# Optimization experiments

Hardware: AMD Instinct MI355X
Metric: run time of the kernel (lower is better)

The kernel has to match this reference:

```python
import jax, jax.numpy as jnp
import numpy as np

B, N, M = 4, 512, 8192
QUERY_DIM, INPUT_DIM = 512, 256
HEADS, DIM_HEAD = 8, 64
ATT_DIM = HEADS * DIM_HEAD  # 512


def setup_inputs() -> dict:
    key = jax.random.key(0)
    ks = jax.random.split(key, 6)
    x = jax.random.normal(ks[0], (B, N, QUERY_DIM), dtype=jnp.float32)
    context = jax.random.normal(ks[1], (B, M, INPUT_DIM), dtype=jnp.float32)
    # Linear weights stored as [in, out] for x @ W
    Wq = jax.random.normal(ks[2], (QUERY_DIM, ATT_DIM), dtype=jnp.float32) / np.sqrt(QUERY_DIM)
    Wkv = jax.random.normal(ks[3], (INPUT_DIM, 2 * ATT_DIM), dtype=jnp.float32) / np.sqrt(INPUT_DIM)
    Wo = jax.random.normal(ks[4], (ATT_DIM, QUERY_DIM), dtype=jnp.float32) / np.sqrt(ATT_DIM)
    bo = jax.random.normal(ks[5], (QUERY_DIM,), dtype=jnp.float32) * 0.01
    return {"x": x, "context": context, "Wq": Wq, "Wkv": Wkv, "Wo": Wo, "bo": bo}


def reference(x, context, Wq, Wkv, Wo, bo):
    scale = DIM_HEAD ** -0.5
    q = x @ Wq                      # [B, N, H*D]
    kv = context @ Wkv              # [B, M, 2*H*D]
    k, v = jnp.split(kv, 2, axis=-1)
    # split heads: b n (h d) -> b h n d
    q = q.reshape(B, N, HEADS, DIM_HEAD).transpose(0, 2, 1, 3)
    k = k.reshape(B, M, HEADS, DIM_HEAD).transpose(0, 2, 1, 3)
    v = v.reshape(B, M, HEADS, DIM_HEAD).transpose(0, 2, 1, 3)
    scores = jnp.einsum('bhid,bhjd->bhij', q, k) * scale  # [B, H, N, M]
    attn = jax.nn.softmax(scores, axis=-1)
    out = jnp.einsum('bhij,bhjd->bhid', attn, v)           # [B, H, N, D]
    out = out.transpose(0, 2, 1, 3).reshape(B, N, ATT_DIM)
    return out @ Wo + bo
```

## Files before the change

### kernel.cpp

```cpp
#include <hip/hip_runtime.h>
#include <hip/hip_bf16.h>
#include <cstdint>

#define NB 4
#define NQ 512
#define NM 8192
#define NH 8
#define DH 64

typedef short bf16x8s __attribute__((ext_vector_type(8)));
typedef float f32x4  __attribute__((ext_vector_type(4)));

static __device__ __forceinline__ short f2bs(float f) {
    unsigned u = __builtin_bit_cast(unsigned, f);
    return (short)(unsigned short)((u + 0x8000u) >> 16);
}
static __device__ __forceinline__ unsigned pk2(float a, float b) {
    unsigned au = __builtin_bit_cast(unsigned, a) + 0x8000u;
    unsigned bu = __builtin_bit_cast(unsigned, b) + 0x8000u;
    return __builtin_amdgcn_perm(bu, au, 0x07060302u);
}

#if __has_builtin(__builtin_amdgcn_exp2f)
static __device__ __forceinline__ float fexp2(float x) { return __builtin_amdgcn_exp2f(x); }
#else
static __device__ __forceinline__ float fexp2(float x) { return exp2f(x); }
#endif

__global__ __launch_bounds__(256) void prep_weights(
    const float* __restrict__ Wq, const float* __restrict__ Wo,
    const float* __restrict__ Wkv,
    short* __restrict__ Wqf, short* __restrict__ Wof, short* __restrict__ Wkvf)
{
    const int t = threadIdx.x;
    const int w = t >> 6, ln = t & 63;
    const int m16 = ln & 15, quad = ln >> 4;
    int f = blockIdx.x * 4 + w;
    const float* src; short* dst; int N, KS, n0, ks;
    if (f < 512)       { src = Wq;  dst = Wqf;  N = 512;  KS = 16; n0 = f >> 4; ks = f & 15; }
    else if (f < 1024) { f -= 512;  src = Wo;  dst = Wof;  N = 512;  KS = 16; n0 = f >> 4; ks = f & 15; }
    else               { f -= 1024; src = Wkv; dst = Wkvf; N = 1024; KS = 8;  n0 = f >> 3; ks = f & 7; }
    const float* sp = src + (size_t)(ks * 32 + quad * 8) * N + n0 * 16 + m16;
    float v[8];
    #pragma unroll
    for (int j = 0; j < 8; ++j) v[j] = sp[(size_t)j * N];
    uint4 pkv = { pk2(v[0],v[1]), pk2(v[2],v[3]), pk2(v[4],v[5]), pk2(v[6],v[7]) };
    *(uint4*)(dst + ((size_t)(n0 * KS + ks) * 64 + ln) * 8) = pkv;
}

__device__ __forceinline__ void proj32_body(
    const float* __restrict__ A, const short* __restrict__ Wf,
    float* __restrict__ C, const float* __restrict__ bias,
    int tm, int tn, char* smemraw)
{
    short* As = (short*)smemraw;

    const int t = threadIdx.x;
    const int w = t >> 6, ln = t & 63;
    const int m16 = ln & 15, quad = ln >> 4;
    const int wm = w >> 1, wn = w & 1;

    const int ar = t >> 3, ac = (t & 7) << 3;

    const float* Ap = A + (size_t)(tm * 32 + ar) * 512 + ac;

    f32x4 acc[2] = {};

    for (int k0 = 0; k0 < 512; k0 += 64) {
        float4 a0 = *(const float4*)(Ap + k0);
        float4 a1 = *(const float4*)(Ap + k0 + 4);
        bf16x8s bfr[2][2];
        #pragma unroll
        for (int ks = 0; ks < 2; ++ks)
            #pragma unroll
            for (int nt = 0; nt < 2; ++nt)
                bfr[ks][nt] = *(const bf16x8s*)(Wf +
                    ((size_t)((tn * 4 + wn * 2 + nt) * 16 + (k0 >> 5) + ks) * 64 + ln) * 8);

        __syncthreads();
        {
            uint4 wa = { pk2(a0.x,a0.y), pk2(a0.z,a0.w), pk2(a1.x,a1.y), pk2(a1.z,a1.w) };
            *(uint4*)&As[ar * 72 + ac] = wa;
        }
        __syncthreads();

        #pragma unroll
        for (int ks = 0; ks < 2; ++ks) {
            bf16x8s af = *(const bf16x8s*)&As[(wm * 16 + m16) * 72 + ks * 32 + quad * 8];
            #pragma unroll
            for (int nt = 0; nt < 2; ++nt)
                acc[nt] = __builtin_amdgcn_mfma_f32_16x16x32_bf16(af, bfr[ks][nt], acc[nt], 0, 0, 0);
        }
    }

    const int row0 = tm * 32 + wm * 16 + quad * 4;
    const int col0 = tn * 64 + wn * 32;
    #pragma unroll
    for (int nt = 0; nt < 2; ++nt) {
        const int col = col0 + nt * 16 + m16;
        const float bb = bias ? bias[col] : 0.f;
        #pragma unroll
        for (int r = 0; r < 4; ++r)
            C[(size_t)(row0 + r) * 512 + col] = acc[nt][r] + bb;
    }
}

__device__ __forceinline__ void kv_body(
    const float* __restrict__ A, const short* __restrict__ Wkvf,
    short* __restrict__ Kf, short* __restrict__ Vf,
    int bid, char* smemraw)
{
    short* As = (short*)smemraw;

    const int t  = threadIdx.x;
    const int tm = bid & 255, tn = bid >> 8;
    const int w  = t >> 6, ln = t & 63;
    const int m16 = ln & 15, quad = ln >> 4;
    const int wm = w & 1, wn = w >> 1;

    const int ar = t >> 3;
    const int ac = (t & 7) << 2;

    const float* Abase = A + (size_t)(tm * 128 + ar) * 256 + ac;

    f32x4 acc[4][4] = {};

    for (int k0 = 0; k0 < 256; k0 += 32) {
        float4 av[4];
        #pragma unroll
        for (int p = 0; p < 4; ++p)
            av[p] = *(const float4*)(Abase + (size_t)p * 32 * 256 + k0);
        bf16x8s bfr[4];
        #pragma unroll
        for (int j = 0; j < 4; ++j)
            bfr[j] = *(const bf16x8s*)(Wkvf +
                ((size_t)((tn * 8 + wn * 4 + j) * 8 + (k0 >> 5)) * 64 + ln) * 8);

        __syncthreads();
        #pragma unroll
        for (int p = 0; p < 4; ++p) {
            uint2 wv = { pk2(av[p].x, av[p].y), pk2(av[p].z, av[p].w) };
            *(uint2*)&As[(p * 32 + ar) * 40 + ac] = wv;
        }
        __syncthreads();

        bf16x8s af[4];
        #pragma unroll
        for (int i = 0; i < 4; ++i)
            af[i] = *(const bf16x8s*)&As[(wm * 64 + i * 16 + m16) * 40 + quad * 8];
        #pragma unroll
        for (int i = 0; i < 4; ++i)
            #pragma unroll
            for (int j = 0; j < 4; ++j)
                acc[i][j] = __builtin_amdgcn_mfma_f32_16x16x32_bf16(af[i], bfr[j], acc[i][j], 0, 0, 0);
    }

    const int col0 = tn * 128 + wn * 64;
    const int row0 = tm * 128 + wm * 64;
    const int b    = row0 >> 13;
    const int mr0  = row0 & (NM - 1);

    if (col0 < 512) {
        const int h = col0 >> 6;
        short* Kp = Kf + (size_t)(b * NH + h) * (NM * DH);
        #pragma unroll
        for (int i = 0; i < 4; ++i)
            #pragma unroll
            for (int j = 0; j < 4; ++j) {
                const int d = j * 16 + m16;
                #pragma unroll
                for (int r = 0; r < 4; ++r) {
                    const int key = mr0 + i * 16 + quad * 4 + r;
                    const int idx = ((key >> 4) * 2 + (d >> 5)) * 512
                                  + (((d >> 3) & 3) * 16 + (key & 15)) * 8 + (d & 7);
                    Kp[idx] = f2bs(acc[i][j][r]);
                }
            }
    } else {
        const int h = (col0 - 512) >> 6;
        short* Vp = Vf + (size_t)(b * NH + h) * (NM * DH);
        #pragma unroll
        for (int i = 0; i < 4; ++i)
            #pragma unroll
            for (int j = 0; j < 4; ++j) {
                const int key0 = mr0 + i * 16 + quad * 4;
                const int idx = (j * 256 + (key0 >> 5)) * 512
                              + ((((key0 >> 3) & 3) * 16 + m16) * 8) + (key0 & 7);
                uint2 pk;
                pk.x = pk2(acc[i][j][0], acc[i][j][1]);
                pk.y = pk2(acc[i][j][2], acc[i][j][3]);
                *(uint2*)(Vp + idx) = pk;
            }
    }
}

__global__ __launch_bounds__(256) void gemm_kvq(
    const float* __restrict__ x,   const short* __restrict__ Wqf, float* __restrict__ q,
    const float* __restrict__ ctx, const short* __restrict__ Wkvf,
    short* __restrict__ Kf, short* __restrict__ Vf)
{
    __shared__ __align__(16) char smem[10240];
    if (blockIdx.x < 512)
        proj32_body(x, Wqf, q, nullptr, (int)(blockIdx.x >> 3), (int)(blockIdx.x & 7), smem);
    else
        kv_body(ctx, Wkvf, Kf, Vf, (int)(blockIdx.x - 512), smem);
}

__global__ __launch_bounds__(256) void gemm_proj32(
    const float* __restrict__ A, const short* __restrict__ Wf,
    float* __restrict__ C, const float* __restrict__ bias)
{
    __shared__ __align__(16) char smem[32 * 72 * 2];
    proj32_body(A, Wf, C, bias, (int)(blockIdx.x >> 3), (int)(blockIdx.x & 7), smem);
}

__global__ __launch_bounds__(512, 2) void attn_mfma(
    const float* __restrict__ Q,
    const short* __restrict__ Kfr,
    const short* __restrict__ Vfr,
    float* __restrict__ Og)
{
    __shared__ __align__(16) float Ob[2][64 * 66];
    __shared__ float lbuf[8 * 64];

    const int bid = blockIdx.x;
    const int xcd = bid & 7, g = bid >> 3;
    const int bh  = xcd * 4 + (g & 3);
    const int qt  = g >> 2;
    const int b   = bh >> 3, h = bh & 7;
    const int t   = threadIdx.x;
    const int w   = t >> 6, ln = t & 63;
    const int m16 = ln & 15, quad = ln >> 4;

    const short* Kbase = Kfr + (size_t)bh * (NM * DH);
    const short* Vbase = Vfr + (size_t)bh * (NM * DH);

    const float qsc = 0.125f * 1.44269504f;
    bf16x8s qf[4][2];
    #pragma unroll
    for (int mt = 0; mt < 4; ++mt) {
        const float* qrow = Q + ((size_t)(b * NQ + qt * 64 + mt * 16 + m16)) * 512 + h * 64;
        #pragma unroll
        for (int ks = 0; ks < 2; ++ks) {
            float4 x0 = *(const float4*)(qrow + ks * 32 + quad * 8);
            float4 x1 = *(const float4*)(qrow + ks * 32 + quad * 8 + 4);
            uint4 pkv = { pk2(x0.x * qsc, x0.y * qsc), pk2(x0.z * qsc, x0.w * qsc),
                          pk2(x1.x * qsc, x1.y * qsc), pk2(x1.z * qsc, x1.w * qsc) };
            qf[mt][ks] = *reinterpret_cast<bf16x8s*>(&pkv);
        }
    }

    bf16x8s ones;
    #pragma unroll
    for (int j = 0; j < 8; ++j) ones[j] = (short)0x3F80;

    f32x4 o[4][4] = {};
    f32x4 lsum[4] = {};

    const int srcLo = (((quad << 1) & 3) << 4) + m16;
    const int srcHi = ((((quad << 1) + 1) & 3) << 4) + m16;
    const bool ktHi = quad >= 2;

    bf16x8s kf[4][2];
    {
        const int kc = w * 64;
        #pragma unroll
        for (int nt = 0; nt < 4; ++nt)
            #pragma unroll
            for (int ks = 0; ks < 2; ++ks)
                kf[nt][ks] = *(const bf16x8s*)(Kbase + ((((kc >> 4) + nt) * 2 + ks) << 9) + ln * 8);
    }

    for (int it = 0; it < 16; ++it) {
        const int kc = it * 512 + w * 64;

        bf16x8s vf[4][2];
        #pragma unroll
        for (int dt = 0; dt < 4; ++dt)
            #pragma unroll
            for (int ks = 0; ks < 2; ++ks)
                vf[dt][ks] = *(const bf16x8s*)(Vbase + ((dt * 256 + (kc >> 5) + ks) << 9) + ln * 8);

        f32x4 st[4][4] = {};
        #pragma unroll
        for (int kt = 0; kt < 4; ++kt)
            #pragma unroll
            for (int mt = 0; mt < 4; ++mt) {
                st[mt][kt] = __builtin_amdgcn_mfma_f32_16x16x32_bf16(kf[kt][0], qf[mt][0], st[mt][kt], 0, 0, 0);
                st[mt][kt] = __builtin_amdgcn_mfma_f32_16x16x32_bf16(kf[kt][1], qf[mt][1], st[mt][kt], 0, 0, 0);
            }

        if (it + 1 < 16) {
            const int kn = (it + 1) * 512 + w * 64;
            #pragma unroll
            for (int nt = 0; nt < 4; ++nt)
                #pragma unroll
                for (int ks = 0; ks < 2; ++ks)
                    kf[nt][ks] = *(const bf16x8s*)(Kbase + ((((kn >> 4) + nt) * 2 + ks) << 9) + ln * 8);
        }

        unsigned pp[4][4][2];
        #pragma unroll
        for (int mt = 0; mt < 4; ++mt)
            #pragma unroll
            for (int kt = 0; kt < 4; ++kt) {
                const float p0 = fexp2(st[mt][kt][0]);
                const float p1 = fexp2(st[mt][kt][1]);
                const float p2 = fexp2(st[mt][kt][2]);
                const float p3 = fexp2(st[mt][kt][3]);
                pp[mt][kt][0] = pk2(p0, p1);
                pp[mt][kt][1] = pk2(p2, p3);
            }

        #pragma unroll
        for (int mt = 0; mt < 4; ++mt)
            #pragma unroll
            for (int ks = 0; ks < 2; ++ks) {
                const unsigned a0 = __shfl(pp[mt][2 * ks][0], srcLo);
                const unsigned b0 = __shfl(pp[mt][2 * ks + 1][0], srcLo);
                const unsigned a1 = __shfl(pp[mt][2 * ks][1], srcLo);
                const unsigned b1 = __shfl(pp[mt][2 * ks + 1][1], srcLo);
                const unsigned a2 = __shfl(pp[mt][2 * ks][0], srcHi);
                const unsigned b2 = __shfl(pp[mt][2 * ks + 1][0], srcHi);
                const unsigned a3 = __shfl(pp[mt][2 * ks][1], srcHi);
                const unsigned b3 = __shfl(pp[mt][2 * ks + 1][1], srcHi);
                uint4 pb;
                pb.x = ktHi ? b0 : a0;
                pb.y = ktHi ? b1 : a1;
                pb.z = ktHi ? b2 : a2;
                pb.w = ktHi ? b3 : a3;
                bf16x8s pbv = *reinterpret_cast<bf16x8s*>(&pb);
                #pragma unroll
                for (int dt = 0; dt < 4; ++dt)
                    o[mt][dt] = __builtin_amdgcn_mfma_f32_16x16x32_bf16(vf[dt][ks], pbv, o[mt][dt], 0, 0, 0);
                lsum[mt] = __builtin_amdgcn_mfma_f32_16x16x32_bf16(ones, pbv, lsum[mt], 0, 0, 0);
            }
    }

    if (quad == 0) {
        #pragma unroll
        for (int mt = 0; mt < 4; ++mt)
            lbuf[w * 64 + mt * 16 + m16] = lsum[mt][0];
    }
    if (w < 2) {
        float* dst = Ob[w];
        #pragma unroll
        for (int mt = 0; mt < 4; ++mt)
            #pragma unroll
            for (int dt = 0; dt < 4; ++dt)
                *(f32x4*)&dst[(mt * 16 + m16) * 66 + dt * 16 + quad * 4] = o[mt][dt];
    }
    __syncthreads();
    #pragma unroll
    for (int ph = 1; ph < 4; ++ph) {
        if ((w >> 1) == ph) {
            float* dst = Ob[w & 1];
            #pragma unroll
            for (int mt = 0; mt < 4; ++mt)
                #pragma unroll
                for (int dt = 0; dt < 4; ++dt) {
                    float* p = &dst[(mt * 16 + m16) * 66 + dt * 16 + quad * 4];
                    f32x4 cur = *(f32x4*)p;
                    cur += o[mt][dt];
                    *(f32x4*)p = cur;
                }
        }
        __syncthreads();
    }
    {
        const int row = t >> 3;
        const int d0  = (t & 7) << 3;
        float l = 0.f;
        #pragma unroll
        for (int wi = 0; wi < 8; ++wi) l += lbuf[wi * 64 + row];
        const float inv = 1.0f / l;
        float* op = Og + ((size_t)(b * NQ + qt * 64 + row)) * 512 + h * 64 + d0;
        #pragma unroll
        for (int j = 0; j < 2; ++j) {
            const int c = row * 66 + d0 + j * 4;
            float4 r;
            r.x = (Ob[0][c + 0] + Ob[1][c + 0]) * inv;
            r.y = (Ob[0][c + 1] + Ob[1][c + 1]) * inv;
            r.z = (Ob[0][c + 2] + Ob[1][c + 2]) * inv;
            r.w = (Ob[0][c + 3] + Ob[1][c + 3]) * inv;
            *(float4*)(op + j * 4) = r;
        }
    }
}

extern "C" void kernel_launch(void* const* d_in, const int* in_sizes, int n_in,
                              void* d_out, int out_size, void* d_ws, size_t ws_size,
                              hipStream_t stream) {
    (void)in_sizes; (void)n_in; (void)out_size; (void)ws_size;

    const float* x   = (const float*)d_in[0];
    const float* ctx = (const float*)d_in[1];
    const float* Wq  = (const float*)d_in[2];
    const float* Wkv = (const float*)d_in[3];
    const float* Wo  = (const float*)d_in[4];
    const float* bo  = (const float*)d_in[5];
    float* out = (float*)d_out;

    float* ws    = (float*)d_ws;
    float* q     = ws;
    float* attno = q + (size_t)2048 * 512;
    short* Kf    = (short*)(attno + (size_t)2048 * 512);
    short* Vf    = Kf + (size_t)NB * NH * NM * DH;
    short* Wqf   = Vf + (size_t)NB * NH * NM * DH;
    short* Wof   = Wqf + (size_t)512 * 512;
    short* Wkvf  = Wof + (size_t)512 * 512;

    prep_weights<<<dim3(384), dim3(256), 0, stream>>>(Wq, Wo, Wkv, Wqf, Wof, Wkvf);

    gemm_kvq<<<dim3(2560), dim3(256), 0, stream>>>(x, Wqf, q, ctx, Wkvf, Kf, Vf);

    attn_mfma<<<dim3(256), dim3(512), 0, stream>>>(q, Kf, Vf, attno);

    gemm_proj32<<<dim3(512), dim3(256), 0, stream>>>(attno, Wof, out, bo);
}
```

Baseline: 189.6 us.

## Rearrange V layout to feed PV MFMAs directly, removing cross-lane shuffles

Changes the V buffer layout written by the KV projection so each lane's 16-bit-aligned score fragment from the QK MFMA output can feed a 16x16x16 bf16 MFMA directly, removing the 16 shuffles and selects per tile in the attention loop. V is stored and loaded as contiguous uint4 per lane, and the KV block index mapping is also reordered. In exchange, the PV product uses twice as many smaller-K MFMA instructions (16x16x16 instead of 16x16x32), which have lower throughput per instruction.

```diff
diff --git a/kernel.cpp b/kernel.cpp
--- a/kernel.cpp
+++ b/kernel.cpp
@@ -9,6 +9,7 @@
 #define DH 64
 
 typedef short bf16x8s __attribute__((ext_vector_type(8)));
+typedef short bf16x4s __attribute__((ext_vector_type(4)));
 typedef float f32x4  __attribute__((ext_vector_type(4)));
 
 static __device__ __forceinline__ short f2bs(float f) {
@@ -108,12 +109,13 @@
 __device__ __forceinline__ void kv_body(
     const float* __restrict__ A, const short* __restrict__ Wkvf,
     short* __restrict__ Kf, short* __restrict__ Vf,
-    int bid, char* smemraw)
+    int kvid, char* smemraw)
 {
     short* As = (short*)smemraw;
 
     const int t  = threadIdx.x;
-    const int tm = bid & 255, tn = bid >> 8;
+    const int tm = ((kvid >> 6) << 3) | (kvid & 7);
+    const int tn = (kvid >> 3) & 7;
     const int w  = t >> 6, ln = t & 63;
     const int m16 = ln & 15, quad = ln >> 4;
     const int wm = w & 1, wn = w >> 1;
@@ -180,16 +182,15 @@
         const int h = (col0 - 512) >> 6;
         short* Vp = Vf + (size_t)(b * NH + h) * (NM * DH);
         #pragma unroll
-        for (int i = 0; i < 4; ++i)
-            #pragma unroll
-            for (int j = 0; j < 4; ++j) {
-                const int key0 = mr0 + i * 16 + quad * 4;
-                const int idx = (j * 256 + (key0 >> 5)) * 512
-                              + ((((key0 >> 3) & 3) * 16 + m16) * 8) + (key0 & 7);
-                uint2 pk;
-                pk.x = pk2(acc[i][j][0], acc[i][j][1]);
-                pk.y = pk2(acc[i][j][2], acc[i][j][3]);
-                *(uint2*)(Vp + idx) = pk;
+        for (int j = 0; j < 4; ++j)
+            #pragma unroll
+            for (int p = 0; p < 2; ++p) {
+                uint4 v;
+                v.x = pk2(acc[2*p    ][j][0], acc[2*p    ][j][1]);
+                v.y = pk2(acc[2*p    ][j][2], acc[2*p    ][j][3]);
+                v.z = pk2(acc[2*p + 1][j][0], acc[2*p + 1][j][1]);
+                v.w = pk2(acc[2*p + 1][j][2], acc[2*p + 1][j][3]);
+                *(uint4*)(Vp + ((size_t)(j * 256 + (mr0 >> 5) + p) * 64 + ln) * 8) = v;
             }
     }
 }
@@ -250,16 +251,12 @@
         }
     }
 
-    bf16x8s ones;
+    bf16x4s ones4;
     #pragma unroll
-    for (int j = 0; j < 8; ++j) ones[j] = (short)0x3F80;
+    for (int j = 0; j < 4; ++j) ones4[j] = (short)0x3F80;
 
     f32x4 o[4][4] = {};
     f32x4 lsum[4] = {};
-
-    const int srcLo = (((quad << 1) & 3) << 4) + m16;
-    const int srcHi = ((((quad << 1) + 1) & 3) << 4) + m16;
-    const bool ktHi = quad >= 2;
 
     bf16x8s kf[4][2];
     {
@@ -274,12 +271,12 @@
     for (int it = 0; it < 16; ++it) {
         const int kc = it * 512 + w * 64;
 
-        bf16x8s vf[4][2];
+        uint4 vraw[4][2];
         #pragma unroll
         for (int dt = 0; dt < 4; ++dt)
             #pragma unroll
-            for (int ks = 0; ks < 2; ++ks)
-                vf[dt][ks] = *(const bf16x8s*)(Vbase + ((dt * 256 + (kc >> 5) + ks) << 9) + ln * 8);
+            for (int kp = 0; kp < 2; ++kp)
+                vraw[dt][kp] = *(const uint4*)(Vbase + ((size_t)(dt * 256 + (kc >> 5) + kp) * 64 + ln) * 8);
 
         f32x4 st[4][4] = {};
         #pragma unroll
@@ -299,7 +296,6 @@
                     kf[nt][ks] = *(const bf16x8s*)(Kbase + ((((kn >> 4) + nt) * 2 + ks) << 9) + ln * 8);
         }
 
-        unsigned pp[4][4][2];
         #pragma unroll
         for (int mt = 0; mt < 4; ++mt)
             #pragma unroll
@@ -308,32 +304,17 @@
                 const float p1 = fexp2(st[mt][kt][1]);
                 const float p2 = fexp2(st[mt][kt][2]);
                 const float p3 = fexp2(st[mt][kt][3]);
-                pp[mt][kt][0] = pk2(p0, p1);
-                pp[mt][kt][1] = pk2(p2, p3);
-            }
-
-        #pragma unroll
-        for (int mt = 0; mt < 4; ++mt)
-            #pragma unroll
-            for (int ks = 0; ks < 2; ++ks) {
-                const unsigned a0 = __shfl(pp[mt][2 * ks][0], srcLo);
-                const unsigned b0 = __shfl(pp[mt][2 * ks + 1][0], srcLo);
-                const unsigned a1 = __shfl(pp[mt][2 * ks][1], srcLo);
-                const unsigned b1 = __shfl(pp[mt][2 * ks + 1][1], srcLo);
-                const unsigned a2 = __shfl(pp[mt][2 * ks][0], srcHi);
-                const unsigned b2 = __shfl(pp[mt][2 * ks + 1][0], srcHi);
-                const unsigned a3 = __shfl(pp[mt][2 * ks][1], srcHi);
-                const unsigned b3 = __shfl(pp[mt][2 * ks + 1][1], srcHi);
-                uint4 pb;
-                pb.x = ktHi ? b0 : a0;
-                pb.y = ktHi ? b1 : a1;
-                pb.z = ktHi ? b2 : a2;
-                pb.w = ktHi ? b3 : a3;
-                bf16x8s pbv = *reinterpret_cast<bf16x8s*>(&pb);
+                uint2 pu = { pk2(p0, p1), pk2(p2, p3) };
+                bf16x4s pbv = *reinterpret_cast<bf16x4s*>(&pu);
+                const int kp = kt >> 1, hh = kt & 1;
                 #pragma unroll
-                for (int dt = 0; dt < 4; ++dt)
-                    o[mt][dt] = __builtin_amdgcn_mfma_f32_16x16x32_bf16(vf[dt][ks], pbv, o[mt][dt], 0, 0, 0);
-                lsum[mt] = __builtin_amdgcn_mfma_f32_16x16x32_bf16(ones, pbv, lsum[mt], 0, 0, 0);
+                for (int dt = 0; dt < 4; ++dt) {
+                    uint2 vh = hh ? make_uint2(vraw[dt][kp].z, vraw[dt][kp].w)
+                                  : make_uint2(vraw[dt][kp].x, vraw[dt][kp].y);
+                    bf16x4s va = *reinterpret_cast<bf16x4s*>(&vh);
+                    o[mt][dt] = __builtin_amdgcn_mfma_f32_16x16x16bf16_1k(va, pbv, o[mt][dt], 0, 0, 0);
+                }
+                lsum[mt] = __builtin_amdgcn_mfma_f32_16x16x16bf16_1k(ones4, pbv, lsum[mt], 0, 0, 0);
             }
     }
 
```

Measured after the change: 186.2 us. Within noise of the previous version (-1.8%).
